# Performance work log

Hardware: AMD Instinct MI355X
Metric: run time of the kernel (lower is better)

## Reference

```python
import jax, jax.numpy as jnp
import numpy as np

B, N, E, ED, H, HID, OUT = 128, 100, 3200, 8, 4, 16, 32


def _ln(x, g, b):
    m = x.mean(-1, keepdims=True)
    v = ((x - m) ** 2).mean(-1, keepdims=True)
    return (x - m) / jnp.sqrt(v + 1e-5) * g + b


def _seg_softmax(logits, seg, n):
    # logits: [Etot, H], seg: [Etot] target node ids
    m = jax.ops.segment_max(logits, seg, num_segments=n)
    ex = jnp.exp(logits - m[seg])
    s = jax.ops.segment_sum(ex, seg, num_segments=n)
    return ex / (s[seg] + 1e-16)


def _tconv(x, src, dst, ea, Wq, bq, Wk, bk, Wv, bv, We, Ws, bs, heads, ch, n):
    # PyG TransformerConv, concat=False, root_weight=True, beta=False
    q = (x @ Wq.T + bq).reshape(-1, heads, ch)
    k = (x @ Wk.T + bk).reshape(-1, heads, ch)
    v = (x @ Wv.T + bv).reshape(-1, heads, ch)
    e = (ea @ We.T).reshape(-1, heads, ch)
    alpha = (q[dst] * (k[src] + e)).sum(-1) / jnp.sqrt(jnp.float32(ch))  # [Etot,H]
    alpha = _seg_softmax(alpha, dst, n)
    msg = (v[src] + e) * alpha[..., None]
    out = jax.ops.segment_sum(msg, dst, num_segments=n)  # [n,H,ch]
    out = out.mean(axis=1)  # concat=False -> head mean
    return out + x @ Ws.T + bs


def setup_inputs() -> dict:
    key = jax.random.key(0)
    ks = jax.random.split(key, 32)
    d = {}
    d['nodes_feats'] = jax.random.randint(ks[0], (B, N, 1), 0, 5).astype(jnp.float32)
    d['edge_index'] = jax.random.randint(ks[1], (B, 2, E), 0, N).astype(jnp.int32)
    d['edge_attr'] = jax.random.normal(ks[2], (B, E, ED), jnp.float32)
    d['agent_id'] = jax.random.randint(ks[3], (B, 1), 0, N).astype(jnp.int32)
    s = 0.1
    d['entity_embed'] = jax.random.normal(ks[4], (5, 4), jnp.float32)
    d['W1'] = jax.random.normal(ks[5], (HID, 4 + ED), jnp.float32) * s
    d['b1'] = jnp.zeros((HID,), jnp.float32)
    d['W2'] = jax.random.normal(ks[6], (HID, HID), jnp.float32) * s
    d['b2'] = jnp.zeros((HID,), jnp.float32)
    d['W3'] = jax.random.normal(ks[7], (HID, HID), jnp.float32) * s
    d['b3'] = jnp.zeros((HID,), jnp.float32)
    d['ln_g'] = jnp.ones((HID,), jnp.float32)
    d['ln_b'] = jnp.zeros((HID,), jnp.float32)
    i = 8
    for pre, ch, outd in (('g1', HID, HID), ('g2', OUT, OUT)):
        d[pre + '_Wq'] = jax.random.normal(ks[i + 0], (H * ch, HID), jnp.float32) * s
        d[pre + '_bq'] = jnp.zeros((H * ch,), jnp.float32)
        d[pre + '_Wk'] = jax.random.normal(ks[i + 1], (H * ch, HID), jnp.float32) * s
        d[pre + '_bk'] = jnp.zeros((H * ch,), jnp.float32)
        d[pre + '_Wv'] = jax.random.normal(ks[i + 2], (H * ch, HID), jnp.float32) * s
        d[pre + '_bv'] = jnp.zeros((H * ch,), jnp.float32)
        d[pre + '_We'] = jax.random.normal(ks[i + 3], (H * ch, ED), jnp.float32) * s
        d[pre + '_Ws'] = jax.random.normal(ks[i + 4], (outd, HID), jnp.float32) * s
        d[pre + '_bs'] = jnp.zeros((outd,), jnp.float32)
        i += 5
    return d


def reference(nodes_feats, edge_index, edge_attr, agent_id, entity_embed,
              W1, b1, W2, b2, W3, b3, ln_g, ln_b,
              g1_Wq, g1_bq, g1_Wk, g1_bk, g1_Wv, g1_bv, g1_We, g1_Ws, g1_bs,
              g2_Wq, g2_bq, g2_Wk, g2_bk, g2_Wv, g2_bv, g2_We, g2_Ws, g2_bs):
    n_tot = B * N
    # batched graph -> flat graph with per-batch node offsets
    offs = (jnp.arange(B, dtype=edge_index.dtype) * N)[:, None, None]
    ei = (edge_index + offs).transpose(1, 0, 2).reshape(2, -1)  # [2, B*E]
    src, dst = ei[0], ei[1]
    x = nodes_feats.reshape(-1, 1)            # [n_tot, 1]
    ea = edge_attr.reshape(-1, ED)            # [B*E, ED]

    # Embedding message-passing layer (aggr='add')
    etype = x[:, 0].astype(jnp.int32)[src]
    emb = entity_embed[etype]                  # [Etot, 4]
    h = jnp.concatenate([emb, ea], axis=1)
    h = _ln(jax.nn.relu(h @ W1.T + b1), ln_g, ln_b)
    h = _ln(jax.nn.relu(h @ W2.T + b2), ln_g, ln_b)
    h = _ln(jax.nn.relu(h @ W3.T + b3), ln_g, ln_b)
    z = jax.ops.segment_sum(h, dst, num_segments=n_tot)  # [n_tot, 16]

    a = _tconv(z, src, dst, ea, g1_Wq, g1_bq, g1_Wk, g1_bk, g1_Wv, g1_bv,
               g1_We, g1_Ws, g1_bs, H, HID, n_tot)
    a = _tconv(a, src, dst, ea, g2_Wq, g2_bq, g2_Wk, g2_bk, g2_Wv, g2_bv,
               g2_We, g2_Ws, g2_bs, H, OUT, n_tot)
    a = jax.nn.relu(a).reshape(B, N, OUT)
    # graph_aggr == 'agent': gather the agent node per batch
    out = jnp.take_along_axis(a, agent_id[:, :, None].astype(jnp.int32), axis=1)
    return out[:, 0, :]  # [B, OUT]
```

## Files before the change

kernel.cpp:

```cpp
#include <hip/hip_runtime.h>
#include <math.h>
#include <stdint.h>

#define Bb   128
#define Nn   100
#define Ee   3200
#define NTOT (Bb*Nn)
#define ETOT (Bb*Ee)



__global__ __launch_bounds__(512) void k_csr(const int* __restrict__ ei,
                                             const int* __restrict__ agent,
                                             int* __restrict__ off,
                                             int2* __restrict__ cpair,
                                             int* __restrict__ mark)
{
    int b = ((blockIdx.x & 7) << 4) + (blockIdx.x >> 3);
    int t = threadIdx.x;
    __shared__ int s_src[Ee];
    __shared__ int s_dst[Ee];
    __shared__ int cnt[128];
    __shared__ int exc[128];
    __shared__ int cur[128];
    if (t < 128) cnt[t] = 0;
    if (t < Nn) mark[b * Nn + t] = 0;
    __syncthreads();
    const int* eis = ei + (size_t)b * 2 * Ee;
    const int* eid = eis + Ee;
    for (int e = t; e < Ee; e += 512) {
        int s = eis[e];
        int d = eid[e];
        s_src[e] = s;
        s_dst[e] = d;
        atomicAdd(&cnt[d], 1);
    }
    __syncthreads();
    if (t < 128) exc[t] = cnt[t];
    __syncthreads();
    for (int d = 1; d < 128; d <<= 1) {
        int v = 0;
        if (t < 128 && t >= d) v = exc[t - d];
        __syncthreads();
        if (t < 128) exc[t] += v;
        __syncthreads();
    }
    if (t < 128) { int e0 = exc[t] - cnt[t]; exc[t] = e0; cur[t] = e0; }
    __syncthreads();
    if (t < Nn) off[b * Nn + t] = b * Ee + exc[t];
    if (b == Bb - 1 && t == 0) off[NTOT] = ETOT;
    for (int e = t; e < Ee; e += 512) {
        int d = s_dst[e];
        int idx = atomicAdd(&cur[d], 1);
        cpair[b * Ee + idx] = make_int2(s_src[e] + b * Nn, b * Ee + e);
    }
    int an = agent[b];
    if (t == 0) mark[b * Nn + an] = 1;
    for (int e = t; e < Ee; e += 512) {
        if (s_dst[e] == an) mark[b * Nn + s_src[e]] = 1;
    }
}


__device__ __forceinline__ void ln_reg(float* h, const float* __restrict__ g,
                                       const float* __restrict__ b) {
    float s = 0.f;
#pragma unroll
    for (int c = 0; c < 16; c++) s += h[c];
    float m = s * 0.0625f;
    float v = 0.f;
#pragma unroll
    for (int c = 0; c < 16; c++) { float d = h[c] - m; v += d * d; }
    float r = rsqrtf(v * 0.0625f + 1e-5f);
#pragma unroll
    for (int c = 0; c < 16; c++) h[c] = (h[c] - m) * r * g[c] + b[c];
}

__global__ __launch_bounds__(256) void k_mlpz(
    const float* __restrict__ nf, const float* __restrict__ ea, const float* __restrict__ ee,
    const float* __restrict__ W1, const float* __restrict__ b1,
    const float* __restrict__ W2, const float* __restrict__ b2,
    const float* __restrict__ W3, const float* __restrict__ b3,
    const float* __restrict__ lg, const float* __restrict__ lb,
    const float* __restrict__ Wk, const float* __restrict__ bk,
    const float* __restrict__ Wv, const float* __restrict__ bv,
    const int* __restrict__ off, const int2* __restrict__ cpair,
    float* __restrict__ z, float* __restrict__ k1, float* __restrict__ v1)
{
    __shared__ float hs[4][64][17];
    __shared__ int sdeg[4];
    int lane = threadIdx.x & 63;
    int wid  = threadIdx.x >> 6;
    int n    = (blockIdx.x & 7) * (NTOT / 8) + (blockIdx.x >> 3) * 4 + wid;

    int o0 = off[n];
    int deg = off[n + 1] - o0;
    if (lane == 0) sdeg[wid] = deg;
    __syncthreads();
    int mdeg = max(max(sdeg[0], sdeg[1]), max(sdeg[2], sdeg[3]));
    int chunks = (mdeg + 63) >> 6;

    float zp = 0.f;
    for (int ch = 0; ch < chunks; ch++) {
        int i = ch * 64 + lane;
        float h3[16];
        if (i < deg) {
            int2 p = cpair[o0 + i];
            int et = (int)nf[p.x];
            float in[12];
#pragma unroll
            for (int j = 0; j < 4; j++) in[j] = ee[et * 4 + j];
            const float4* ea4 = (const float4*)(ea + (size_t)p.y * 8);
            float4 ua = ea4[0], ub = ea4[1];
            in[4] = ua.x; in[5] = ua.y; in[6] = ua.z; in[7] = ua.w;
            in[8] = ub.x; in[9] = ub.y; in[10] = ub.z; in[11] = ub.w;

            float h1[16];
#pragma unroll
            for (int c = 0; c < 16; c++) {
                float s = b1[c];
#pragma unroll
                for (int j = 0; j < 12; j++) s = fmaf(W1[c * 12 + j], in[j], s);
                h1[c] = fmaxf(s, 0.f);
            }
            ln_reg(h1, lg, lb);
            float h2[16];
#pragma unroll
            for (int c = 0; c < 16; c++) {
                float s = b2[c];
#pragma unroll
                for (int j = 0; j < 16; j++) s = fmaf(W2[c * 16 + j], h1[j], s);
                h2[c] = fmaxf(s, 0.f);
            }
            ln_reg(h2, lg, lb);
#pragma unroll
            for (int c = 0; c < 16; c++) {
                float s = b3[c];
#pragma unroll
                for (int j = 0; j < 16; j++) s = fmaf(W3[c * 16 + j], h2[j], s);
                h3[c] = fmaxf(s, 0.f);
            }
            ln_reg(h3, lg, lb);
        } else {
#pragma unroll
            for (int c = 0; c < 16; c++) h3[c] = 0.f;
        }
#pragma unroll
        for (int c = 0; c < 16; c++) hs[wid][lane][c] = h3[c];
        __syncthreads();
        int g = lane >> 4, c = lane & 15;
        float s = 0.f;
#pragma unroll
        for (int k = 0; k < 16; k++) s += hs[wid][g * 16 + k][c];
        s += __shfl_xor(s, 16);
        s += __shfl_xor(s, 32);
        zp += s;
        __syncthreads();
    }

    if (lane < 16) z[n * 16 + lane] = zp;

    float ak = bk[lane], av = bv[lane];
#pragma unroll
    for (int j = 0; j < 16; j++) {
        float zj = __shfl(zp, j, 16);
        ak = fmaf(Wk[lane * 16 + j], zj, ak);
        av = fmaf(Wv[lane * 16 + j], zj, av);
    }
    k1[n * 64 + lane] = ak;
    v1[n * 64 + lane] = av;
}


__global__ __launch_bounds__(512) void k_attn(
    const float* __restrict__ ea,
    const float* __restrict__ k1, const float* __restrict__ v1,
    const float* __restrict__ z, const int* __restrict__ mark,
    const int* __restrict__ agent,
    const int* __restrict__ off, const int2* __restrict__ cpair,
    const float* __restrict__ g1Wq, const float* __restrict__ g1bq,
    const float* __restrict__ g1We, const float* __restrict__ g1Ws, const float* __restrict__ g1bs,
    const float* __restrict__ g2Wq, const float* __restrict__ g2bq,
    const float* __restrict__ g2Wk, const float* __restrict__ g2bk,
    const float* __restrict__ g2Wv, const float* __restrict__ g2bv,
    const float* __restrict__ g2We, const float* __restrict__ g2Ws, const float* __restrict__ g2bs,
    float* __restrict__ out)
{
    __shared__ alignas(16) float sk[Nn][64];
    __shared__ alignas(16) float sv[Nn][64];
    __shared__ alignas(16) int2  spair[Ee];
    __shared__ alignas(16) float sz[Nn][16];
    __shared__ float a1s[Nn][16];
    __shared__ int   soff[Nn + 1];
    __shared__ int   smark[Nn];
    __shared__ float sm2[8][64], sl2[8][64], sa0[8][64], sa1[8][64];

    int b = ((blockIdx.x & 7) << 4) + (blockIdx.x >> 3);
    int t = threadIdx.x;
    int lane = t & 63;
    int wid  = t >> 6;

    const float4* kg = (const float4*)(k1 + (size_t)b * Nn * 64);
    const float4* vg = (const float4*)(v1 + (size_t)b * Nn * 64);
    const float4* zg = (const float4*)(z  + (size_t)b * Nn * 16);
    float4* skd = (float4*)&sk[0][0];
    float4* svd = (float4*)&sv[0][0];
    float4* szd = (float4*)&sz[0][0];
    for (int i = t; i < Nn * 16; i += 512) { skd[i] = kg[i]; svd[i] = vg[i]; }
    for (int i = t; i < Nn * 4; i += 512) szd[i] = zg[i];
    const int2* cg = cpair + (size_t)b * Ee;
    for (int i = t; i < Ee; i += 512) spair[i] = cg[i];
    if (t <= Nn) soff[t] = off[b * Nn + t] - b * Ee;
    if (t < Nn) smark[t] = mark[b * Nn + t];
    __syncthreads();

    float wq[16], wer[8], ws1[16];
#pragma unroll
    for (int j = 0; j < 16; j++) wq[j] = g1Wq[lane * 16 + j];
#pragma unroll
    for (int j = 0; j < 8; j++) wer[j] = g1We[lane * 8 + j];
    float bq1 = g1bq[lane];
    int lc = lane & 15;
#pragma unroll
    for (int j = 0; j < 16; j++) ws1[j] = g1Ws[lc * 16 + j];
    float bs1 = g1bs[lc];

    for (int loc = wid; loc < Nn; loc += 8) {
        if (!smark[loc]) continue;
        float zz[16];
#pragma unroll
        for (int j = 0; j < 16; j++) zz[j] = sz[loc][j];
        float ql = bq1;
#pragma unroll
        for (int j = 0; j < 16; j++) ql = fmaf(wq[j], zz[j], ql);

        int o0 = soff[loc];
        int deg = soff[loc + 1] - o0;

        float m = -1e30f, l = 0.f, acc = 0.f;
        int i = 0;
        for (; i + 2 <= deg; i += 2) {
            int2 pA = spair[o0 + i];
            int2 pB = spair[o0 + i + 1];
            const float4* eaA = (const float4*)(ea + (size_t)pA.y * 8);
            const float4* eaB = (const float4*)(ea + (size_t)pB.y * 8);
            float4 a0v = eaA[0], a1v = eaA[1], b0v = eaB[0], b1v = eaB[1];
            float eA = wer[0] * a0v.x + wer[1] * a0v.y + wer[2] * a0v.z + wer[3] * a0v.w
                     + wer[4] * a1v.x + wer[5] * a1v.y + wer[6] * a1v.z + wer[7] * a1v.w;
            float eB = wer[0] * b0v.x + wer[1] * b0v.y + wer[2] * b0v.z + wer[3] * b0v.w
                     + wer[4] * b1v.x + wer[5] * b1v.y + wer[6] * b1v.z + wer[7] * b1v.w;
            int la = pA.x - b * Nn, lB = pB.x - b * Nn;
            float kA = sk[la][lane], kB = sk[lB][lane];
            float vA = sv[la][lane], vB = sv[lB][lane];
            float tA = ql * (kA + eA);
            float tB = ql * (kB + eB);
            tA += __shfl_xor(tA, 1, 16);  tB += __shfl_xor(tB, 1, 16);
            tA += __shfl_xor(tA, 2, 16);  tB += __shfl_xor(tB, 2, 16);
            tA += __shfl_xor(tA, 4, 16);  tB += __shfl_xor(tB, 4, 16);
            tA += __shfl_xor(tA, 8, 16);  tB += __shfl_xor(tB, 8, 16);
            float lA = tA * 0.25f;
            float lBv = tB * 0.25f;
            float nm = fmaxf(m, fmaxf(lA, lBv));
            float sc = __expf(m - nm);
            float wA = __expf(lA - nm);
            float wB = __expf(lBv - nm);
            acc = acc * sc + wA * (vA + eA) + wB * (vB + eB);
            l   = l * sc + wA + wB;
            m   = nm;
        }
        for (; i < deg; i++) {
            int2 p = spair[o0 + i];
            const float4* ea4 = (const float4*)(ea + (size_t)p.y * 8);
            float4 u0 = ea4[0], u1 = ea4[1];
            float el = wer[0] * u0.x + wer[1] * u0.y + wer[2] * u0.z + wer[3] * u0.w
                     + wer[4] * u1.x + wer[5] * u1.y + wer[6] * u1.z + wer[7] * u1.w;
            int ls = p.x - b * Nn;
            float kl = sk[ls][lane];
            float tq = ql * (kl + el);
            tq += __shfl_xor(tq, 1, 16);
            tq += __shfl_xor(tq, 2, 16);
            tq += __shfl_xor(tq, 4, 16);
            tq += __shfl_xor(tq, 8, 16);
            float logit = tq * 0.25f;
            float nm = fmaxf(m, logit);
            float sc = __expf(m - nm);
            float w  = __expf(logit - nm);
            float vl = sv[ls][lane];
            acc = acc * sc + w * (vl + el);
            l   = l * sc + w;
            m   = nm;
        }
        float y = (deg > 0) ? (acc / l) : 0.f;
        y += __shfl_xor(y, 16);
        y += __shfl_xor(y, 32);
        y *= 0.25f;
        if (lane < 16) {
            float r = bs1;
#pragma unroll
            for (int j = 0; j < 16; j++) r = fmaf(ws1[j], zz[j], r);
            a1s[loc][lane] = y + r;
        }
    }
    __syncthreads();

    int an = agent[b];
    int v0 = lane * 2, v1i = lane * 2 + 1;

    float aa[16];
#pragma unroll
    for (int j = 0; j < 16; j++) aa[j] = a1s[an][j];

    float wk0[16], wk1[16], wv0[16], wv1[16], we0[8], we1[8];
#pragma unroll
    for (int j = 0; j < 16; j++) {
        wk0[j] = g2Wk[v0 * 16 + j];  wk1[j] = g2Wk[v1i * 16 + j];
        wv0[j] = g2Wv[v0 * 16 + j];  wv1[j] = g2Wv[v1i * 16 + j];
    }
#pragma unroll
    for (int j = 0; j < 8; j++) { we0[j] = g2We[v0 * 8 + j]; we1[j] = g2We[v1i * 8 + j]; }

    float q0 = g2bq[v0], q1v = g2bq[v1i];
#pragma unroll
    for (int j = 0; j < 16; j++) {
        q0  = fmaf(g2Wq[v0 * 16 + j],  aa[j], q0);
        q1v = fmaf(g2Wq[v1i * 16 + j], aa[j], q1v);
    }

    int o0a = soff[an];
    int dega = soff[an + 1] - o0a;

    float m = -1e30f, l = 0.f, a0 = 0.f, a1c = 0.f;
    for (int i = wid; i < dega; i += 8) {
        int2 p = spair[o0a + i];
        int srcl = p.x - b * Nn;
        float as[16];
#pragma unroll
        for (int j = 0; j < 16; j++) as[j] = a1s[srcl][j];
        const float4* ea4 = (const float4*)(ea + (size_t)p.y * 8);
        float4 u0 = ea4[0], u1 = ea4[1];
        float eav[8] = {u0.x, u0.y, u0.z, u0.w, u1.x, u1.y, u1.z, u1.w};

        float k0 = g2bk[v0], k1v = g2bk[v1i], vv0 = g2bv[v0], vv1 = g2bv[v1i];
#pragma unroll
        for (int j = 0; j < 16; j++) {
            k0  = fmaf(wk0[j], as[j], k0);
            k1v = fmaf(wk1[j], as[j], k1v);
            vv0 = fmaf(wv0[j], as[j], vv0);
            vv1 = fmaf(wv1[j], as[j], vv1);
        }
        float e0 = 0.f, e1 = 0.f;
#pragma unroll
        for (int j = 0; j < 8; j++) { e0 = fmaf(we0[j], eav[j], e0); e1 = fmaf(we1[j], eav[j], e1); }

        float tq = q0 * (k0 + e0) + q1v * (k1v + e1);
        tq += __shfl_xor(tq, 1, 16);
        tq += __shfl_xor(tq, 2, 16);
        tq += __shfl_xor(tq, 4, 16);
        tq += __shfl_xor(tq, 8, 16);
        float logit = tq * 0.17677669529663687f;
        float nm = fmaxf(m, logit);
        float sc = __expf(m - nm);
        float wgt = __expf(logit - nm);
        a0  = a0 * sc + wgt * (vv0 + e0);
        a1c = a1c * sc + wgt * (vv1 + e1);
        l   = l * sc + wgt;
        m   = nm;
    }
    sm2[wid][lane] = m; sl2[wid][lane] = l; sa0[wid][lane] = a0; sa1[wid][lane] = a1c;
    __syncthreads();
    if (wid == 0) {
        float M = sm2[0][lane];
#pragma unroll
        for (int ww = 1; ww < 8; ww++) M = fmaxf(M, sm2[ww][lane]);
        float L = 0.f, A0 = 0.f, A1 = 0.f;
#pragma unroll
        for (int ww = 0; ww < 8; ww++) {
            float sc = __expf(sm2[ww][lane] - M);
            L  += sc * sl2[ww][lane];
            A0 += sc * sa0[ww][lane];
            A1 += sc * sa1[ww][lane];
        }
        float y0 = (dega > 0) ? (A0 / L) : 0.f;
        float y1 = (dega > 0) ? (A1 / L) : 0.f;
        y0 += __shfl_xor(y0, 16); y0 += __shfl_xor(y0, 32);
        y1 += __shfl_xor(y1, 16); y1 += __shfl_xor(y1, 32);
        y0 *= 0.25f; y1 *= 0.25f;

        if (lane < 16) {
            int c0 = lane * 2, c1 = lane * 2 + 1;
            float r0 = g2bs[c0], r1 = g2bs[c1];
#pragma unroll
            for (int j = 0; j < 16; j++) {
                r0 = fmaf(g2Ws[c0 * 16 + j], aa[j], r0);
                r1 = fmaf(g2Ws[c1 * 16 + j], aa[j], r1);
            }
            out[b * 32 + c0] = fmaxf(y0 + r0, 0.f);
            out[b * 32 + c1] = fmaxf(y1 + r1, 0.f);
        }
    }
}


extern "C" void kernel_launch(void* const* d_in, const int* in_sizes, int n_in,
                              void* d_out, int out_size, void* d_ws, size_t ws_size,
                              hipStream_t stream) {
    (void)in_sizes; (void)n_in; (void)out_size; (void)ws_size;
    const float* nf    = (const float*)d_in[0];
    const int*   ei    = (const int*)d_in[1];
    const float* ea    = (const float*)d_in[2];
    const int*   agent = (const int*)d_in[3];
    const float* ee    = (const float*)d_in[4];
    const float* W1    = (const float*)d_in[5];
    const float* b1    = (const float*)d_in[6];
    const float* W2    = (const float*)d_in[7];
    const float* b2    = (const float*)d_in[8];
    const float* W3    = (const float*)d_in[9];
    const float* b3    = (const float*)d_in[10];
    const float* lg    = (const float*)d_in[11];
    const float* lb    = (const float*)d_in[12];
    const float* g1Wq  = (const float*)d_in[13];
    const float* g1bq  = (const float*)d_in[14];
    const float* g1Wk  = (const float*)d_in[15];
    const float* g1bk  = (const float*)d_in[16];
    const float* g1Wv  = (const float*)d_in[17];
    const float* g1bv  = (const float*)d_in[18];
    const float* g1We  = (const float*)d_in[19];
    const float* g1Ws  = (const float*)d_in[20];
    const float* g1bs  = (const float*)d_in[21];
    const float* g2Wq  = (const float*)d_in[22];
    const float* g2bq  = (const float*)d_in[23];
    const float* g2Wk  = (const float*)d_in[24];
    const float* g2bk  = (const float*)d_in[25];
    const float* g2Wv  = (const float*)d_in[26];
    const float* g2bv  = (const float*)d_in[27];
    const float* g2We  = (const float*)d_in[28];
    const float* g2Ws  = (const float*)d_in[29];
    const float* g2bs  = (const float*)d_in[30];
    float* out = (float*)d_out;

    char* w = (char*)d_ws;
    int* mark  = (int*)w;  w += (size_t)NTOT * 4;
    int* off   = (int*)w;  w += (size_t)(NTOT + 4) * 4;
    w = (char*)(((uintptr_t)w + 15) & ~(uintptr_t)15);
    int2* cpair = (int2*)w; w += (size_t)ETOT * 8;
    float* z   = (float*)w; w += (size_t)NTOT * 16 * 4;
    float* k1  = (float*)w; w += (size_t)NTOT * 64 * 4;
    float* v1  = (float*)w; w += (size_t)NTOT * 64 * 4;

    k_csr<<<dim3(Bb), dim3(512), 0, stream>>>(ei, agent, off, cpair, mark);
    k_mlpz<<<dim3(NTOT / 4), dim3(256), 0, stream>>>(
        nf, ea, ee, W1, b1, W2, b2, W3, b3, lg, lb,
        g1Wk, g1bk, g1Wv, g1bv,
        off, cpair, z, k1, v1);
    k_attn<<<dim3(Bb), dim3(512), 0, stream>>>(
        ea, k1, v1, z, mark, agent, off, cpair,
        g1Wq, g1bq, g1We, g1Ws, g1bs,
        g2Wq, g2bq, g2Wk, g2bk, g2Wv, g2bv, g2We, g2Ws, g2bs,
        out);
}
```

Before: 236.3 us.

## Fuse CSR build, edge MLP and attention into one per-graph kernel

Merges the three kernels into a single 1024-thread block per graph. CSR, node embeddings and layer-1 keys and values are now built in shared memory instead of global workspace. This removes two launches and the global round-trips for the intermediate arrays, and the marked-node list avoids scanning unmarked nodes. In exchange, the edge MLP runs on only one block per graph instead of thousands of blocks, which sharply reduces parallelism across the GPU.

```diff
diff --git a/kernel.cpp b/kernel.cpp
--- a/kernel.cpp
+++ b/kernel.cpp
@@ -5,61 +5,6 @@
 #define Bb   128
 #define Nn   100
 #define Ee   3200
-#define NTOT (Bb*Nn)
-#define ETOT (Bb*Ee)
-
-
-
-__global__ __launch_bounds__(512) void k_csr(const int* __restrict__ ei,
-                                             const int* __restrict__ agent,
-                                             int* __restrict__ off,
-                                             int2* __restrict__ cpair,
-                                             int* __restrict__ mark)
-{
-    int b = ((blockIdx.x & 7) << 4) + (blockIdx.x >> 3);
-    int t = threadIdx.x;
-    __shared__ int s_src[Ee];
-    __shared__ int s_dst[Ee];
-    __shared__ int cnt[128];
-    __shared__ int exc[128];
-    __shared__ int cur[128];
-    if (t < 128) cnt[t] = 0;
-    if (t < Nn) mark[b * Nn + t] = 0;
-    __syncthreads();
-    const int* eis = ei + (size_t)b * 2 * Ee;
-    const int* eid = eis + Ee;
-    for (int e = t; e < Ee; e += 512) {
-        int s = eis[e];
-        int d = eid[e];
-        s_src[e] = s;
-        s_dst[e] = d;
-        atomicAdd(&cnt[d], 1);
-    }
-    __syncthreads();
-    if (t < 128) exc[t] = cnt[t];
-    __syncthreads();
-    for (int d = 1; d < 128; d <<= 1) {
-        int v = 0;
-        if (t < 128 && t >= d) v = exc[t - d];
-        __syncthreads();
-        if (t < 128) exc[t] += v;
-        __syncthreads();
-    }
-    if (t < 128) { int e0 = exc[t] - cnt[t]; exc[t] = e0; cur[t] = e0; }
-    __syncthreads();
-    if (t < Nn) off[b * Nn + t] = b * Ee + exc[t];
-    if (b == Bb - 1 && t == 0) off[NTOT] = ETOT;
-    for (int e = t; e < Ee; e += 512) {
-        int d = s_dst[e];
-        int idx = atomicAdd(&cur[d], 1);
-        cpair[b * Ee + idx] = make_int2(s_src[e] + b * Nn, b * Ee + e);
-    }
-    int an = agent[b];
-    if (t == 0) mark[b * Nn + an] = 1;
-    for (int e = t; e < Ee; e += 512) {
-        if (s_dst[e] == an) mark[b * Nn + s_src[e]] = 1;
-    }
-}
 
 
 __device__ __forceinline__ void ln_reg(float* h, const float* __restrict__ g,
@@ -76,109 +21,17 @@
     for (int c = 0; c < 16; c++) h[c] = (h[c] - m) * r * g[c] + b[c];
 }
 
-__global__ __launch_bounds__(256) void k_mlpz(
-    const float* __restrict__ nf, const float* __restrict__ ea, const float* __restrict__ ee,
+__global__ __launch_bounds__(1024) void k_fused(
+    const float* __restrict__ nf, const int* __restrict__ ei,
+    const float* __restrict__ ea, const int* __restrict__ agent,
+    const float* __restrict__ ee,
     const float* __restrict__ W1, const float* __restrict__ b1,
     const float* __restrict__ W2, const float* __restrict__ b2,
     const float* __restrict__ W3, const float* __restrict__ b3,
     const float* __restrict__ lg, const float* __restrict__ lb,
-    const float* __restrict__ Wk, const float* __restrict__ bk,
-    const float* __restrict__ Wv, const float* __restrict__ bv,
-    const int* __restrict__ off, const int2* __restrict__ cpair,
-    float* __restrict__ z, float* __restrict__ k1, float* __restrict__ v1)
-{
-    __shared__ float hs[4][64][17];
-    __shared__ int sdeg[4];
-    int lane = threadIdx.x & 63;
-    int wid  = threadIdx.x >> 6;
-    int n    = (blockIdx.x & 7) * (NTOT / 8) + (blockIdx.x >> 3) * 4 + wid;
-
-    int o0 = off[n];
-    int deg = off[n + 1] - o0;
-    if (lane == 0) sdeg[wid] = deg;
-    __syncthreads();
-    int mdeg = max(max(sdeg[0], sdeg[1]), max(sdeg[2], sdeg[3]));
-    int chunks = (mdeg + 63) >> 6;
-
-    float zp = 0.f;
-    for (int ch = 0; ch < chunks; ch++) {
-        int i = ch * 64 + lane;
-        float h3[16];
-        if (i < deg) {
-            int2 p = cpair[o0 + i];
-            int et = (int)nf[p.x];
-            float in[12];
-#pragma unroll
-            for (int j = 0; j < 4; j++) in[j] = ee[et * 4 + j];
-            const float4* ea4 = (const float4*)(ea + (size_t)p.y * 8);
-            float4 ua = ea4[0], ub = ea4[1];
-            in[4] = ua.x; in[5] = ua.y; in[6] = ua.z; in[7] = ua.w;
-            in[8] = ub.x; in[9] = ub.y; in[10] = ub.z; in[11] = ub.w;
-
-            float h1[16];
-#pragma unroll
-            for (int c = 0; c < 16; c++) {
-                float s = b1[c];
-#pragma unroll
-                for (int j = 0; j < 12; j++) s = fmaf(W1[c * 12 + j], in[j], s);
-                h1[c] = fmaxf(s, 0.f);
-            }
-            ln_reg(h1, lg, lb);
-            float h2[16];
-#pragma unroll
-            for (int c = 0; c < 16; c++) {
-                float s = b2[c];
-#pragma unroll
-                for (int j = 0; j < 16; j++) s = fmaf(W2[c * 16 + j], h1[j], s);
-                h2[c] = fmaxf(s, 0.f);
-            }
-            ln_reg(h2, lg, lb);
-#pragma unroll
-            for (int c = 0; c < 16; c++) {
-                float s = b3[c];
-#pragma unroll
-                for (int j = 0; j < 16; j++) s = fmaf(W3[c * 16 + j], h2[j], s);
-                h3[c] = fmaxf(s, 0.f);
-            }
-            ln_reg(h3, lg, lb);
-        } else {
-#pragma unroll
-            for (int c = 0; c < 16; c++) h3[c] = 0.f;
-        }
-#pragma unroll
-        for (int c = 0; c < 16; c++) hs[wid][lane][c] = h3[c];
-        __syncthreads();
-        int g = lane >> 4, c = lane & 15;
-        float s = 0.f;
-#pragma unroll
-        for (int k = 0; k < 16; k++) s += hs[wid][g * 16 + k][c];
-        s += __shfl_xor(s, 16);
-        s += __shfl_xor(s, 32);
-        zp += s;
-        __syncthreads();
-    }
-
-    if (lane < 16) z[n * 16 + lane] = zp;
-
-    float ak = bk[lane], av = bv[lane];
-#pragma unroll
-    for (int j = 0; j < 16; j++) {
-        float zj = __shfl(zp, j, 16);
-        ak = fmaf(Wk[lane * 16 + j], zj, ak);
-        av = fmaf(Wv[lane * 16 + j], zj, av);
-    }
-    k1[n * 64 + lane] = ak;
-    v1[n * 64 + lane] = av;
-}
-
-
-__global__ __launch_bounds__(512) void k_attn(
-    const float* __restrict__ ea,
-    const float* __restrict__ k1, const float* __restrict__ v1,
-    const float* __restrict__ z, const int* __restrict__ mark,
-    const int* __restrict__ agent,
-    const int* __restrict__ off, const int2* __restrict__ cpair,
     const float* __restrict__ g1Wq, const float* __restrict__ g1bq,
+    const float* __restrict__ g1Wk, const float* __restrict__ g1bk,
+    const float* __restrict__ g1Wv, const float* __restrict__ g1bv,
     const float* __restrict__ g1We, const float* __restrict__ g1Ws, const float* __restrict__ g1bs,
     const float* __restrict__ g2Wq, const float* __restrict__ g2bq,
     const float* __restrict__ g2Wk, const float* __restrict__ g2bk,
@@ -186,32 +39,149 @@
     const float* __restrict__ g2We, const float* __restrict__ g2Ws, const float* __restrict__ g2bs,
     float* __restrict__ out)
 {
-    __shared__ alignas(16) float sk[Nn][64];
-    __shared__ alignas(16) float sv[Nn][64];
-    __shared__ alignas(16) int2  spair[Ee];
-    __shared__ alignas(16) float sz[Nn][16];
-    __shared__ float a1s[Nn][16];
+    __shared__ int   s_src[Ee];
+    __shared__ int   s_dst[Ee];
+    __shared__ int2  spair[Ee];
+    __shared__ float sk[Nn][64];
+    __shared__ float sv[Nn][64];
+    __shared__ float sz[Nn][16];
+    __shared__ float sa1[Nn][16];
+    __shared__ float rm[16][64], rl[16][64], r0[16][64], r1[16][64];
+    __shared__ int   cnt[128], exc2[128], cur[128];
     __shared__ int   soff[Nn + 1];
     __shared__ int   smark[Nn];
-    __shared__ float sm2[8][64], sl2[8][64], sa0[8][64], sa1[8][64];
-
-    int b = ((blockIdx.x & 7) << 4) + (blockIdx.x >> 3);
+    __shared__ int   sml[Nn];
+    __shared__ int   smcnt;
+
+    int b = blockIdx.x;
     int t = threadIdx.x;
     int lane = t & 63;
-    int wid  = t >> 6;
-
-    const float4* kg = (const float4*)(k1 + (size_t)b * Nn * 64);
-    const float4* vg = (const float4*)(v1 + (size_t)b * Nn * 64);
-    const float4* zg = (const float4*)(z  + (size_t)b * Nn * 16);
-    float4* skd = (float4*)&sk[0][0];
-    float4* svd = (float4*)&sv[0][0];
-    float4* szd = (float4*)&sz[0][0];
-    for (int i = t; i < Nn * 16; i += 512) { skd[i] = kg[i]; svd[i] = vg[i]; }
-    for (int i = t; i < Nn * 4; i += 512) szd[i] = zg[i];
-    const int2* cg = cpair + (size_t)b * Ee;
-    for (int i = t; i < Ee; i += 512) spair[i] = cg[i];
-    if (t <= Nn) soff[t] = off[b * Nn + t] - b * Ee;
-    if (t < Nn) smark[t] = mark[b * Nn + t];
+    int w    = t >> 6;
+
+    const int* eis = ei + (size_t)b * 2 * Ee;
+    const int* eid = eis + Ee;
+    if (t < 128) cnt[t] = 0;
+    if (t < Nn)  smark[t] = 0;
+    if (t == 0)  smcnt = 0;
+    __syncthreads();
+    for (int e = t; e < Ee; e += 1024) {
+        int s = eis[e];
+        int d = eid[e];
+        s_src[e] = s;
+        s_dst[e] = d;
+        atomicAdd(&cnt[d], 1);
+    }
+    __syncthreads();
+    if (t < 128) exc2[t] = cnt[t];
+    __syncthreads();
+    for (int dd = 1; dd < 128; dd <<= 1) {
+        int v = 0;
+        if (t < 128 && t >= dd) v = exc2[t - dd];
+        __syncthreads();
+        if (t < 128) exc2[t] += v;
+        __syncthreads();
+    }
+    if (t < 128) { int e0 = exc2[t] - cnt[t]; cur[t] = e0; if (t < Nn) soff[t] = e0; }
+    if (t == 0) soff[Nn] = Ee;
+    __syncthreads();
+    for (int e = t; e < Ee; e += 1024) {
+        int d = s_dst[e];
+        int idx = atomicAdd(&cur[d], 1);
+        spair[idx] = make_int2(s_src[e], e);
+    }
+    int an = agent[b];
+    if (t == 0) {
+        int old = atomicExch(&smark[an], 1);
+        if (!old) { int ix = atomicAdd(&smcnt, 1); sml[ix] = an; }
+    }
+    for (int e = t; e < Ee; e += 1024) {
+        if (s_dst[e] == an) {
+            int s = s_src[e];
+            int old = atomicExch(&smark[s], 1);
+            if (!old) { int ix = atomicAdd(&smcnt, 1); sml[ix] = s; }
+        }
+    }
+    __syncthreads();
+
+    int lane32 = t & 31;
+    int grp    = t >> 5;
+    const float* eab = ea + (size_t)b * Ee * 8;
+    for (int n0 = grp; n0 < Nn; n0 += 32) {
+        int o0  = soff[n0];
+        int deg = soff[n0 + 1] - o0;
+        float zs[16];
+#pragma unroll
+        for (int c = 0; c < 16; c++) zs[c] = 0.f;
+        int chunks = (deg + 31) >> 5;
+        for (int ch = 0; ch < chunks; ch++) {
+            int i = ch * 32 + lane32;
+            float h3[16];
+            if (i < deg) {
+                int2 p = spair[o0 + i];
+                int et = (int)nf[b * Nn + p.x];
+                float in[12];
+#pragma unroll
+                for (int j = 0; j < 4; j++) in[j] = ee[et * 4 + j];
+                const float4* ea4 = (const float4*)(eab + (size_t)p.y * 8);
+                float4 ua = ea4[0], ub = ea4[1];
+                in[4] = ua.x; in[5] = ua.y; in[6] = ua.z; in[7] = ua.w;
+                in[8] = ub.x; in[9] = ub.y; in[10] = ub.z; in[11] = ub.w;
+
+                float h1[16];
+#pragma unroll
+                for (int c = 0; c < 16; c++) {
+                    float s = b1[c];
+#pragma unroll
+                    for (int j = 0; j < 12; j++) s = fmaf(W1[c * 12 + j], in[j], s);
+                    h1[c] = fmaxf(s, 0.f);
+                }
+                ln_reg(h1, lg, lb);
+                float h2[16];
+#pragma unroll
+                for (int c = 0; c < 16; c++) {
+                    float s = b2[c];
+#pragma unroll
+                    for (int j = 0; j < 16; j++) s = fmaf(W2[c * 16 + j], h1[j], s);
+                    h2[c] = fmaxf(s, 0.f);
+                }
+                ln_reg(h2, lg, lb);
+#pragma unroll
+                for (int c = 0; c < 16; c++) {
+                    float s = b3[c];
+#pragma unroll
+                    for (int j = 0; j < 16; j++) s = fmaf(W3[c * 16 + j], h2[j], s);
+                    h3[c] = fmaxf(s, 0.f);
+                }
+                ln_reg(h3, lg, lb);
+            } else {
+#pragma unroll
+                for (int c = 0; c < 16; c++) h3[c] = 0.f;
+            }
+#pragma unroll
+            for (int c = 0; c < 16; c++) {
+                float s = h3[c];
+                s += __shfl_xor(s, 1, 32);
+                s += __shfl_xor(s, 2, 32);
+                s += __shfl_xor(s, 4, 32);
+                s += __shfl_xor(s, 8, 32);
+                s += __shfl_xor(s, 16, 32);
+                zs[c] += s;
+            }
+        }
+#pragma unroll
+        for (int c = 0; c < 16; c++) if (lane32 == c) sz[n0][c] = zs[c];
+        int c0 = lane32, c1 = lane32 + 32;
+        float k0 = g1bk[c0], k1v = g1bk[c1], v0 = g1bv[c0], v1v = g1bv[c1];
+#pragma unroll
+        for (int j = 0; j < 16; j++) {
+            k0  = fmaf(g1Wk[c0 * 16 + j], zs[j], k0);
+            k1v = fmaf(g1Wk[c1 * 16 + j], zs[j], k1v);
+            v0  = fmaf(g1Wv[c0 * 16 + j], zs[j], v0);
+            v1v = fmaf(g1Wv[c1 * 16 + j], zs[j], v1v);
+        }
+        sk[n0][c0] = k0;  sk[n0][c1] = k1v;
+        sv[n0][c0] = v0;  sv[n0][c1] = v1v;
+    }
     __syncthreads();
 
     float wq[16], wer[8], ws1[16];
@@ -219,134 +189,125 @@
     for (int j = 0; j < 16; j++) wq[j] = g1Wq[lane * 16 + j];
 #pragma unroll
     for (int j = 0; j < 8; j++) wer[j] = g1We[lane * 8 + j];
-    float bq1 = g1bq[lane];
     int lc = lane & 15;
 #pragma unroll
     for (int j = 0; j < 16; j++) ws1[j] = g1Ws[lc * 16 + j];
-    float bs1 = g1bs[lc];
-
-    for (int loc = wid; loc < Nn; loc += 8) {
-        if (!smark[loc]) continue;
-        float zz[16];
-#pragma unroll
-        for (int j = 0; j < 16; j++) zz[j] = sz[loc][j];
+    float bq1 = g1bq[lane], bs1 = g1bs[lc];
+
+    int nm = smcnt;
+    for (int ix = w; ix < nm; ix += 16) {
+        int n0 = sml[ix];
+        float zfrag = sz[n0][lane & 15];
         float ql = bq1;
 #pragma unroll
-        for (int j = 0; j < 16; j++) ql = fmaf(wq[j], zz[j], ql);
-
-        int o0 = soff[loc];
-        int deg = soff[loc + 1] - o0;
+        for (int j = 0; j < 16; j++) ql = fmaf(wq[j], __shfl(zfrag, j, 16), ql);
+
+        int o0  = soff[n0];
+        int deg = soff[n0 + 1] - o0;
 
         float m = -1e30f, l = 0.f, acc = 0.f;
         int i = 0;
         for (; i + 2 <= deg; i += 2) {
             int2 pA = spair[o0 + i];
             int2 pB = spair[o0 + i + 1];
-            const float4* eaA = (const float4*)(ea + (size_t)pA.y * 8);
-            const float4* eaB = (const float4*)(ea + (size_t)pB.y * 8);
+            const float4* eaA = (const float4*)(eab + (size_t)pA.y * 8);
+            const float4* eaB = (const float4*)(eab + (size_t)pB.y * 8);
             float4 a0v = eaA[0], a1v = eaA[1], b0v = eaB[0], b1v = eaB[1];
             float eA = wer[0] * a0v.x + wer[1] * a0v.y + wer[2] * a0v.z + wer[3] * a0v.w
                      + wer[4] * a1v.x + wer[5] * a1v.y + wer[6] * a1v.z + wer[7] * a1v.w;
             float eB = wer[0] * b0v.x + wer[1] * b0v.y + wer[2] * b0v.z + wer[3] * b0v.w
                      + wer[4] * b1v.x + wer[5] * b1v.y + wer[6] * b1v.z + wer[7] * b1v.w;
-            int la = pA.x - b * Nn, lB = pB.x - b * Nn;
-            float kA = sk[la][lane], kB = sk[lB][lane];
-            float vA = sv[la][lane], vB = sv[lB][lane];
+            float kA = sk[pA.x][lane], kB = sk[pB.x][lane];
+            float vA = sv[pA.x][lane], vB = sv[pB.x][lane];
             float tA = ql * (kA + eA);
             float tB = ql * (kB + eB);
             tA += __shfl_xor(tA, 1, 16);  tB += __shfl_xor(tB, 1, 16);
             tA += __shfl_xor(tA, 2, 16);  tB += __shfl_xor(tB, 2, 16);
             tA += __shfl_xor(tA, 4, 16);  tB += __shfl_xor(tB, 4, 16);
             tA += __shfl_xor(tA, 8, 16);  tB += __shfl_xor(tB, 8, 16);
-            float lA = tA * 0.25f;
+            float lA  = tA * 0.25f;
             float lBv = tB * 0.25f;
-            float nm = fmaxf(m, fmaxf(lA, lBv));
-            float sc = __expf(m - nm);
-            float wA = __expf(lA - nm);
-            float wB = __expf(lBv - nm);
+            float nmv = fmaxf(m, fmaxf(lA, lBv));
+            float sc = __expf(m - nmv);
+            float wA = __expf(lA - nmv);
+            float wB = __expf(lBv - nmv);
             acc = acc * sc + wA * (vA + eA) + wB * (vB + eB);
             l   = l * sc + wA + wB;
-            m   = nm;
+            m   = nmv;
         }
         for (; i < deg; i++) {
             int2 p = spair[o0 + i];
-            const float4* ea4 = (const float4*)(ea + (size_t)p.y * 8);
+            const float4* ea4 = (const float4*)(eab + (size_t)p.y * 8);
             float4 u0 = ea4[0], u1 = ea4[1];
             float el = wer[0] * u0.x + wer[1] * u0.y + wer[2] * u0.z + wer[3] * u0.w
                      + wer[4] * u1.x + wer[5] * u1.y + wer[6] * u1.z + wer[7] * u1.w;
-            int ls = p.x - b * Nn;
-            float kl = sk[ls][lane];
+            float kl = sk[p.x][lane];
             float tq = ql * (kl + el);
             tq += __shfl_xor(tq, 1, 16);
             tq += __shfl_xor(tq, 2, 16);
             tq += __shfl_xor(tq, 4, 16);
             tq += __shfl_xor(tq, 8, 16);
             float logit = tq * 0.25f;
-            float nm = fmaxf(m, logit);
-            float sc = __expf(m - nm);
-            float w  = __expf(logit - nm);
-            float vl = sv[ls][lane];
-            acc = acc * sc + w * (vl + el);
-            l   = l * sc + w;
-            m   = nm;
+            float nmv = fmaxf(m, logit);
+            float sc = __expf(m - nmv);
+            float wv = __expf(logit - nmv);
+            float vl = sv[p.x][lane];
+            acc = acc * sc + wv * (vl + el);
+            l   = l * sc + wv;
+            m   = nmv;
         }
         float y = (deg > 0) ? (acc / l) : 0.f;
         y += __shfl_xor(y, 16);
         y += __shfl_xor(y, 32);
         y *= 0.25f;
-        if (lane < 16) {
-            float r = bs1;
-#pragma unroll
-            for (int j = 0; j < 16; j++) r = fmaf(ws1[j], zz[j], r);
-            a1s[loc][lane] = y + r;
-        }
-    }
-    __syncthreads();
-
-    int an = agent[b];
-    int v0 = lane * 2, v1i = lane * 2 + 1;
-
+        float r = bs1;
+#pragma unroll
+        for (int j = 0; j < 16; j++) r = fmaf(ws1[j], __shfl(zfrag, j, 16), r);
+        if (lane < 16) sa1[n0][lane] = y + r;
+    }
+    __syncthreads();
+
+    int v0c = lane * 2, v1c = lane * 2 + 1;
+    float aafrag = sa1[an][lane & 15];
     float aa[16];
 #pragma unroll
-    for (int j = 0; j < 16; j++) aa[j] = a1s[an][j];
+    for (int j = 0; j < 16; j++) aa[j] = __shfl(aafrag, j, 16);
 
     float wk0[16], wk1[16], wv0[16], wv1[16], we0[8], we1[8];
 #pragma unroll
     for (int j = 0; j < 16; j++) {
-        wk0[j] = g2Wk[v0 * 16 + j];  wk1[j] = g2Wk[v1i * 16 + j];
-        wv0[j] = g2Wv[v0 * 16 + j];  wv1[j] = g2Wv[v1i * 16 + j];
-    }
-#pragma unroll
-    for (int j = 0; j < 8; j++) { we0[j] = g2We[v0 * 8 + j]; we1[j] = g2We[v1i * 8 + j]; }
-
-    float q0 = g2bq[v0], q1v = g2bq[v1i];
+        wk0[j] = g2Wk[v0c * 16 + j];  wk1[j] = g2Wk[v1c * 16 + j];
+        wv0[j] = g2Wv[v0c * 16 + j];  wv1[j] = g2Wv[v1c * 16 + j];
+    }
+#pragma unroll
+    for (int j = 0; j < 8; j++) { we0[j] = g2We[v0c * 8 + j]; we1[j] = g2We[v1c * 8 + j]; }
+
+    float q0 = g2bq[v0c], q1v = g2bq[v1c];
 #pragma unroll
     for (int j = 0; j < 16; j++) {
-        q0  = fmaf(g2Wq[v0 * 16 + j],  aa[j], q0);
-        q1v = fmaf(g2Wq[v1i * 16 + j], aa[j], q1v);
-    }
-
-    int o0a = soff[an];
+        q0  = fmaf(g2Wq[v0c * 16 + j], aa[j], q0);
+        q1v = fmaf(g2Wq[v1c * 16 + j], aa[j], q1v);
+    }
+
+    int o0a  = soff[an];
     int dega = soff[an + 1] - o0a;
 
-    float m = -1e30f, l = 0.f, a0 = 0.f, a1c = 0.f;
-    for (int i = wid; i < dega; i += 8) {
+    float m2 = -1e30f, l2 = 0.f, a0 = 0.f, a1c = 0.f;
+    for (int i = w; i < dega; i += 16) {
         int2 p = spair[o0a + i];
-        int srcl = p.x - b * Nn;
-        float as[16];
-#pragma unroll
-        for (int j = 0; j < 16; j++) as[j] = a1s[srcl][j];
-        const float4* ea4 = (const float4*)(ea + (size_t)p.y * 8);
+        float asfrag = sa1[p.x][lane & 15];
+        const float4* ea4 = (const float4*)(eab + (size_t)p.y * 8);
         float4 u0 = ea4[0], u1 = ea4[1];
         float eav[8] = {u0.x, u0.y, u0.z, u0.w, u1.x, u1.y, u1.z, u1.w};
 
-        float k0 = g2bk[v0], k1v = g2bk[v1i], vv0 = g2bv[v0], vv1 = g2bv[v1i];
+        float k0 = g2bk[v0c], k1v = g2bk[v1c], vv0 = g2bv[v0c], vv1 = g2bv[v1c];
 #pragma unroll
         for (int j = 0; j < 16; j++) {
-            k0  = fmaf(wk0[j], as[j], k0);
-            k1v = fmaf(wk1[j], as[j], k1v);
-            vv0 = fmaf(wv0[j], as[j], vv0);
-            vv1 = fmaf(wv1[j], as[j], vv1);
+            float asj = __shfl(asfrag, j, 16);
+            k0  = fmaf(wk0[j], asj, k0);
+            k1v = fmaf(wk1[j], asj, k1v);
+            vv0 = fmaf(wv0[j], asj, vv0);
+            vv1 = fmaf(wv1[j], asj, vv1);
         }
         float e0 = 0.f, e1 = 0.f;
 #pragma unroll
@@ -358,27 +319,27 @@
         tq += __shfl_xor(tq, 4, 16);
         tq += __shfl_xor(tq, 8, 16);
         float logit = tq * 0.17677669529663687f;
-        float nm = fmaxf(m, logit);
-        float sc = __expf(m - nm);
-        float wgt = __expf(logit - nm);
+        float nmv = fmaxf(m2, logit);
+        float sc = __expf(m2 - nmv);
+        float wgt = __expf(logit - nmv);
         a0  = a0 * sc + wgt * (vv0 + e0);
         a1c = a1c * sc + wgt * (vv1 + e1);
-        l   = l * sc + wgt;
-        m   = nm;
-    }
-    sm2[wid][lane] = m; sl2[wid][lane] = l; sa0[wid][lane] = a0; sa1[wid][lane] = a1c;
-    __syncthreads();
-    if (wid == 0) {
-        float M = sm2[0][lane];
-#pragma unroll
-        for (int ww = 1; ww < 8; ww++) M = fmaxf(M, sm2[ww][lane]);
+        l2  = l2 * sc + wgt;
+        m2  = nmv;
+    }
+    rm[w][lane] = m2; rl[w][lane] = l2; r0[w][lane] = a0; r1[w][lane] = a1c;
+    __syncthreads();
+    if (w == 0) {
+        float M = rm[0][lane];
+#pragma unroll
+        for (int ww = 1; ww < 16; ww++) M = fmaxf(M, rm[ww][lane]);
         float L = 0.f, A0 = 0.f, A1 = 0.f;
 #pragma unroll
-        for (int ww = 0; ww < 8; ww++) {
-            float sc = __expf(sm2[ww][lane] - M);
-            L  += sc * sl2[ww][lane];
-            A0 += sc * sa0[ww][lane];
-            A1 += sc * sa1[ww][lane];
+        for (int ww = 0; ww < 16; ww++) {
+            float sc = __expf(rm[ww][lane] - M);
+            L  += sc * rl[ww][lane];
+            A0 += sc * r0[ww][lane];
+            A1 += sc * r1[ww][lane];
         }
         float y0 = (dega > 0) ? (A0 / L) : 0.f;
         float y1 = (dega > 0) ? (A1 / L) : 0.f;
@@ -388,14 +349,14 @@
 
         if (lane < 16) {
             int c0 = lane * 2, c1 = lane * 2 + 1;
-            float r0 = g2bs[c0], r1 = g2bs[c1];
+            float rr0 = g2bs[c0], rr1 = g2bs[c1];
 #pragma unroll
             for (int j = 0; j < 16; j++) {
-                r0 = fmaf(g2Ws[c0 * 16 + j], aa[j], r0);
-                r1 = fmaf(g2Ws[c1 * 16 + j], aa[j], r1);
+                rr0 = fmaf(g2Ws[c0 * 16 + j], aa[j], rr0);
+                rr1 = fmaf(g2Ws[c1 * 16 + j], aa[j], rr1);
             }
-            out[b * 32 + c0] = fmaxf(y0 + r0, 0.f);
-            out[b * 32 + c1] = fmaxf(y1 + r1, 0.f);
+            out[b * 32 + c0] = fmaxf(y0 + rr0, 0.f);
+            out[b * 32 + c1] = fmaxf(y1 + rr1, 0.f);
         }
     }
 }
@@ -404,7 +365,7 @@
 extern "C" void kernel_launch(void* const* d_in, const int* in_sizes, int n_in,
                               void* d_out, int out_size, void* d_ws, size_t ws_size,
                               hipStream_t stream) {
-    (void)in_sizes; (void)n_in; (void)out_size; (void)ws_size;
+    (void)in_sizes; (void)n_in; (void)out_size; (void)d_ws; (void)ws_size;
     const float* nf    = (const float*)d_in[0];
     const int*   ei    = (const int*)d_in[1];
     const float* ea    = (const float*)d_in[2];
@@ -438,23 +399,10 @@
     const float* g2bs  = (const float*)d_in[30];
     float* out = (float*)d_out;
 
-    char* w = (char*)d_ws;
-    int* mark  = (int*)w;  w += (size_t)NTOT * 4;
-    int* off   = (int*)w;  w += (size_t)(NTOT + 4) * 4;
-    w = (char*)(((uintptr_t)w + 15) & ~(uintptr_t)15);
-    int2* cpair = (int2*)w; w += (size_t)ETOT * 8;
-    float* z   = (float*)w; w += (size_t)NTOT * 16 * 4;
-    float* k1  = (float*)w; w += (size_t)NTOT * 64 * 4;
-    float* v1  = (float*)w; w += (size_t)NTOT * 64 * 4;
-
-    k_csr<<<dim3(Bb), dim3(512), 0, stream>>>(ei, agent, off, cpair, mark);
-    k_mlpz<<<dim3(NTOT / 4), dim3(256), 0, stream>>>(
-        nf, ea, ee, W1, b1, W2, b2, W3, b3, lg, lb,
-        g1Wk, g1bk, g1Wv, g1bv,
-        off, cpair, z, k1, v1);
-    k_attn<<<dim3(Bb), dim3(512), 0, stream>>>(
-        ea, k1, v1, z, mark, agent, off, cpair,
-        g1Wq, g1bq, g1We, g1Ws, g1bs,
+    k_fused<<<dim3(Bb), dim3(1024), 0, stream>>>(
+        nf, ei, ea, agent, ee,
+        W1, b1, W2, b2, W3, b3, lg, lb,
+        g1Wq, g1bq, g1Wk, g1bk, g1Wv, g1bv, g1We, g1Ws, g1bs,
         g2Wq, g2bq, g2Wk, g2bk, g2Wv, g2bv, g2We, g2Ws, g2bs,
         out);
 }
```

Result: slower. 241.8 us (+2.3%).
